# Performance work log

Measured on AMD Instinct MI355X. Metric: run time of the kernel, lower is better.

The kernel has to match this reference:

```python
import jax, jax.numpy as jnp
import numpy as np

B, S, D, H = 1, 2048, 1024, 16
DH = D // H  # 64
HID = 4 * D
EPS = 1e-5
NEG = -1.0e9


def setup_inputs() -> dict:
    key = jax.random.key(0)
    ks = jax.random.split(key, 12)
    s = 0.02
    return {
        "y": jax.random.normal(ks[0], (B, S, D), jnp.float32),
        "encoder_output": jax.random.normal(ks[1], (B, S, D), jnp.float32),
        # per-head shared projection (query_fc used for q,k,v — faithful to source bug)
        "Wq_self": jax.random.normal(ks[2], (H, D, DH), jnp.float32) * s,
        "bq_self": jax.random.normal(ks[3], (H, DH), jnp.float32) * s,
        "Wq_cross": jax.random.normal(ks[4], (H, D, DH), jnp.float32) * s,
        "bq_cross": jax.random.normal(ks[5], (H, DH), jnp.float32) * s,
        "g1": jnp.ones((D,), jnp.float32), "beta1": jnp.zeros((D,), jnp.float32),
        "g2": jnp.ones((D,), jnp.float32), "beta2": jnp.zeros((D,), jnp.float32),
        "g3": jnp.ones((D,), jnp.float32), "beta3": jnp.zeros((D,), jnp.float32),
        "w1": jax.random.normal(ks[6], (D, HID), jnp.float32) * s,
        "b1": jax.random.normal(ks[7], (HID,), jnp.float32) * s,
        "w2": jax.random.normal(ks[8], (HID, D), jnp.float32) * s,
        "b2": jax.random.normal(ks[9], (D,), jnp.float32) * s,
    }


def _layernorm(x, g, b):
    mu = jnp.mean(x, axis=-1, keepdims=True)
    var = jnp.mean((x - mu) ** 2, axis=-1, keepdims=True)
    return (x - mu) * jax.lax.rsqrt(var + EPS) * g + b


def _mha(x_q, x_kv, W, bias, causal):
    # source bug: q, k, v all use query_fc projection
    q = jnp.einsum('bsd,hde->bhse', x_q, W) + bias[None, :, None, :]
    k = jnp.einsum('bsd,hde->bhse', x_kv, W) + bias[None, :, None, :]
    v = jnp.einsum('bsd,hde->bhse', x_kv, W) + bias[None, :, None, :]
    scores = jnp.einsum('bhse,bhte->bhst', q, k) / jnp.sqrt(jnp.float32(DH))
    if causal:
        sq, sk = scores.shape[-2], scores.shape[-1]
        mask = jnp.triu(jnp.ones((sq, sk), bool), k=1)
        scores = jnp.where(mask, NEG, scores)
    p = jax.nn.softmax(scores, axis=-1)
    out = jnp.einsum('bhst,bhte->bhse', p, v)  # [B,H,S,DH]
    b, h, s, e = out.shape
    return out.transpose(0, 2, 1, 3).reshape(b, s, h * e)


def reference(y, encoder_output, Wq_self, bq_self, Wq_cross, bq_cross,
              g1, beta1, g2, beta2, g3, beta3, w1, b1, w2, b2):
    sa = _mha(y, y, Wq_self, bq_self, causal=True)
    y1 = _layernorm(y + sa, g1, beta1)
    ca = _mha(y1, encoder_output, Wq_cross, bq_cross, causal=False)
    y2 = _layernorm(y1 + ca, g2, beta2)
    ff = jnp.maximum(y2 @ w1 + b1, 0.0) @ w2 + b2
    return _layernorm(y2 + ff, g3, beta3)
```

## Files before the change

kernel.cpp:

```cpp
#include <hip/hip_runtime.h>
#include <hip/hip_bf16.h>


#define S_LEN 2048
#define DMODEL 1024
#define NHEAD 16
#define DHEAD 64
#define HIDDEN 4096

using bf16 = __hip_bfloat16;
typedef __attribute__((ext_vector_type(8))) short bf16x8;
typedef __attribute__((ext_vector_type(4))) float floatx4;

__device__ __forceinline__ void async_ld16(const void* g, void* l) {
  __builtin_amdgcn_global_load_lds(
      (const __attribute__((address_space(1))) unsigned int*)g,
      (__attribute__((address_space(3))) unsigned int*)l, 16, 0, 0);
}

__device__ __forceinline__ unsigned short f2bf_bits(float f) {
  __hip_bfloat16 b = __float2bfloat16(f);
  return *(unsigned short*)&b;
}

template <bool HEADB>
__global__ __launch_bounds__(256) void transp_bf16_kernel(
    const float* __restrict__ src0, bf16* __restrict__ dst0,
    const float* __restrict__ src1, bf16* __restrict__ dst1, int K, int N) {
  const float* src = blockIdx.z ? src1 : src0;
  bf16* dst = blockIdx.z ? dst1 : dst0;
  __shared__ float tile[32][33];
  const int tx = threadIdx.x & 31, ty = threadIdx.x >> 5;
  const int k0 = blockIdx.y * 32, n0 = blockIdx.x * 32;
#pragma unroll
  for (int i = 0; i < 4; ++i) {
    const int k = k0 + ty + i * 8;
    const int n = n0 + tx;
    size_t idx;
    if (HEADB)
      idx = (size_t)(n >> 6) * ((size_t)K * 64) + (size_t)k * 64 + (n & 63);
    else
      idx = (size_t)k * N + n;
    tile[ty + i * 8][tx] = src[idx];
  }
  __syncthreads();
#pragma unroll
  for (int i = 0; i < 4; ++i) {
    const int n = n0 + ty + i * 8;
    const int k = k0 + tx;
    dst[(size_t)n * K + k] = __float2bfloat16(tile[tx][ty + i * 8]);
  }
}

__global__ __launch_bounds__(256) void conv_bf16_kernel(
    const float* __restrict__ src0, bf16* __restrict__ dst0,
    const float* __restrict__ src1, bf16* __restrict__ dst1, int n4) {
  const float* src = blockIdx.z ? src1 : src0;
  bf16* dst = blockIdx.z ? dst1 : dst0;
  const int i = blockIdx.x * 256 + threadIdx.x;
  if (i >= n4) return;
  float4 v = ((const float4*)src)[i];
  unsigned short r[4] = {f2bf_bits(v.x), f2bf_bits(v.y), f2bf_bits(v.z), f2bf_bits(v.w)};
  ((ushort2*)dst)[i * 2] = make_ushort2(r[0], r[1]);
  ((ushort2*)dst)[i * 2 + 1] = make_ushort2(r[2], r[3]);
}

template <int BM, int BN, bool RELU, bool DUALT, typename CT>
__global__ __launch_bounds__(256) void mfma_gemm_kernel(
    const bf16* __restrict__ A0, const bf16* __restrict__ Bt0,
    const float* __restrict__ bias0, CT* __restrict__ C0,
    bf16* __restrict__ Ct0,
    const bf16* __restrict__ A1, const bf16* __restrict__ Bt1,
    const float* __restrict__ bias1, CT* __restrict__ C1,
    bf16* __restrict__ Ct1,
    int M, int N, int Kstride, int Klen) {
  const bf16* A = blockIdx.z ? A1 : A0;
  const bf16* Bt = blockIdx.z ? Bt1 : Bt0;
  const float* bias = blockIdx.z ? bias1 : bias0;
  CT* C = blockIdx.z ? C1 : C0;
  bf16* Ct = blockIdx.z ? Ct1 : Ct0;

  constexpr int MF = (BM + 31) / 32;
  constexpr int NF = BN / 32;
  __shared__ __align__(16) bf16 As[2][BM * 64];
  __shared__ __align__(16) bf16 Bs[2][BN * 64];

  const int tid = threadIdx.x;
  const int wave = tid >> 6;
  const int lane = tid & 63;
  const int m0 = blockIdx.y * BM;
  const int n0 = blockIdx.x * BN;
  const int wr = wave >> 1, wc = wave & 1;

  const int srow = tid >> 3;
  const int schunk = (tid & 7) ^ (srow & 7);
  const bf16* agp = A + (size_t)(m0 + srow) * Kstride + schunk * 8;
  const bf16* bgp = Bt + (size_t)(n0 + srow) * Kstride + schunk * 8;

  floatx4 acc[MF][NF];
#pragma unroll
  for (int i = 0; i < MF; ++i)
#pragma unroll
    for (int j = 0; j < NF; ++j) acc[i][j] = floatx4{0.f, 0.f, 0.f, 0.f};

  const int mrow = lane & 15;
  const int p0 = (((lane >> 4) ^ (mrow & 7)) << 4);
  const int p1 = p0 ^ 64;

  auto stage = [&](int buf, int kt) {
    char* al = (char*)As + buf * (BM * 128) + wave * 1024;
    char* bl = (char*)Bs + buf * (BN * 128) + wave * 1024;
#pragma unroll
    for (int i = 0; i < BM / 32; ++i)
      async_ld16(agp + (size_t)(32 * i) * Kstride + kt, al + i * 4096);
#pragma unroll
    for (int i = 0; i < BN / 32; ++i)
      async_ld16(bgp + (size_t)(32 * i) * Kstride + kt, bl + i * 4096);
  };

  stage(0, 0);
  __syncthreads();

  int cur = 0;
  for (int kt = 0; kt < Klen; kt += 64) {
    const char* abase = (const char*)As + cur * (BM * 128);
    const char* bbase = (const char*)Bs + cur * (BN * 128);
    bf16x8 af0[MF], af1[MF], bf0[NF], bf1[NF];
#pragma unroll
    for (int fi = 0; fi < MF; ++fi) {
      const char* ar = abase + (wr * (BM / 2) + fi * 16 + mrow) * 128;
      af0[fi] = *(const bf16x8*)(ar + p0);
      af1[fi] = *(const bf16x8*)(ar + p1);
    }
#pragma unroll
    for (int fj = 0; fj < NF; ++fj) {
      const char* br = bbase + (wc * (BN / 2) + fj * 16 + mrow) * 128;
      bf0[fj] = *(const bf16x8*)(br + p0);
      bf1[fj] = *(const bf16x8*)(br + p1);
    }

    if (kt + 64 < Klen) stage(cur ^ 1, kt + 64);

#pragma unroll
    for (int fi = 0; fi < MF; ++fi)
#pragma unroll
      for (int fj = 0; fj < NF; ++fj) {
        acc[fi][fj] = __builtin_amdgcn_mfma_f32_16x16x32_bf16(
            af0[fi], bf0[fj], acc[fi][fj], 0, 0, 0);
        acc[fi][fj] = __builtin_amdgcn_mfma_f32_16x16x32_bf16(
            af1[fi], bf1[fj], acc[fi][fj], 0, 0, 0);
      }

    __syncthreads();
    cur ^= 1;
  }

  const int erow = (lane >> 4) * 4;
  const int ecol = lane & 15;
#pragma unroll
  for (int fi = 0; fi < MF; ++fi) {
#pragma unroll
    for (int fj = 0; fj < NF; ++fj) {
      const int nn = n0 + wc * (BN / 2) + fj * 16 + ecol;
      const float bv = bias ? bias[nn] : 0.0f;
      const int mmb = m0 + wr * (BM / 2) + fi * 16 + erow;
      float v[4];
#pragma unroll
      for (int r = 0; r < 4; ++r) {
        v[r] = acc[fi][fj][r] + bv;
        if (RELU) v[r] = fmaxf(v[r], 0.0f);
        if constexpr (sizeof(CT) == 2)
          C[(size_t)(mmb + r) * N + nn] = (CT)__float2bfloat16(v[r]);
        else
          C[(size_t)(mmb + r) * N + nn] = (CT)v[r];
      }
      if (DUALT) {
        ushort4 pk;
        pk.x = f2bf_bits(v[0]);
        pk.y = f2bf_bits(v[1]);
        pk.z = f2bf_bits(v[2]);
        pk.w = f2bf_bits(v[3]);
        *(ushort4*)&Ct[(size_t)nn * M + mmb] = pk;
      }
    }
  }
}

__global__ __launch_bounds__(256) void mfma_attn_kernel(
    const bf16* __restrict__ Q, const bf16* __restrict__ K,
    const bf16* __restrict__ Vt,
    float* __restrict__ OA, float* __restrict__ OB,
    float* __restrict__ LA, float* __restrict__ LB, int causal) {
  __shared__ __align__(16) unsigned short Kt[2][32 * 64];
  __shared__ __align__(16) unsigned short Vs[2][64 * 32];
  __shared__ __align__(16) unsigned short Ps[4][512];

  const int tid = threadIdx.x;
  const int w = tid >> 6, lane = tid & 63;
  const int g = lane >> 4, c = lane & 15;
  const int h = blockIdx.y;
  const int qb = causal ? ((int)gridDim.x - 1 - (int)blockIdx.x)
                        : (int)blockIdx.x;
  const int q0 = qb * 64;
  const int z = blockIdx.z;
  const int qw = q0 + w * 16;
  float* Oz = z ? OB : OA;
  float* Lz = z ? LB : LA;

  const bf16* qrow = Q + (size_t)(qw + c) * DMODEL + h * DHEAD + g * 8;
  const bf16x8 qfa = *(const bf16x8*)qrow;
  const bf16x8 qfb = *(const bf16x8*)(qrow + 32);

  const int srk = tid >> 3;
  const int sck = (tid & 7) ^ (srk & 7);
  const bf16* kgp = K + (size_t)srk * DMODEL + h * DHEAD + sck * 8;
  const int srv = tid >> 2;
  const int scv = (tid & 3) ^ ((srv >> 1) & 3);
  const bf16* vgp = Vt + (size_t)(h * DHEAD + srv) * S_LEN + scv * 8;

  const int kpos0 = ((g ^ (c & 7)) << 4);
  const int kpos1 = kpos0 ^ 64;
  const int vpos = ((g ^ ((c >> 1) & 3)) << 4);
  char* pswave = (char*)Ps + w * 1024;

  floatx4 of[4];
#pragma unroll
  for (int md = 0; md < 4; ++md) of[md] = floatx4{0.f, 0.f, 0.f, 0.f};
  float lpart = 0.f;

  const int nkt = causal ? (q0 / 32 + 2) : (S_LEN / 32);

  auto stage = [&](int buf, int kt) {
    const int t0 = kt * 32;
    async_ld16(kgp + (size_t)t0 * DMODEL, (char*)Kt + buf * 4096 + w * 1024);
    async_ld16(vgp + t0, (char*)Vs + buf * 4096 + w * 1024);
  };

  stage(0, z);
  __syncthreads();

  int cur = 0;
  for (int kt = z; kt < nkt; kt += 2) {
    const int t0 = kt * 32;
    const bool act = !(causal && t0 >= qw + 16);

    bf16x8 kf00, kf01, kf10, kf11, vf0, vf1, vf2, vf3;
    if (act) {
      const char* kbase = (const char*)Kt + cur * 4096;
      const char* vbase = (const char*)Vs + cur * 4096;
      const char* kr0 = kbase + c * 128;
      const char* kr1 = kbase + (16 + c) * 128;
      kf00 = *(const bf16x8*)(kr0 + kpos0);
      kf01 = *(const bf16x8*)(kr0 + kpos1);
      kf10 = *(const bf16x8*)(kr1 + kpos0);
      kf11 = *(const bf16x8*)(kr1 + kpos1);
      vf0 = *(const bf16x8*)(vbase + (c)*64 + vpos);
      vf1 = *(const bf16x8*)(vbase + (16 + c) * 64 + vpos);
      vf2 = *(const bf16x8*)(vbase + (32 + c) * 64 + vpos);
      vf3 = *(const bf16x8*)(vbase + (48 + c) * 64 + vpos);
    }

    if (kt + 2 < nkt) stage(cur ^ 1, kt + 2);

    if (act) {
      const bool diag = causal && (t0 + 32 > qw);
#pragma unroll
      for (int jt = 0; jt < 2; ++jt) {
        floatx4 s = floatx4{0.f, 0.f, 0.f, 0.f};
        __builtin_amdgcn_s_setprio(1);
        s = __builtin_amdgcn_mfma_f32_16x16x32_bf16(jt ? kf10 : kf00, qfa, s, 0, 0, 0);
        s = __builtin_amdgcn_mfma_f32_16x16x32_bf16(jt ? kf11 : kf01, qfb, s, 0, 0, 0);
        __builtin_amdgcn_s_setprio(0);

        ushort4 pk;
        unsigned short* pp = (unsigned short*)&pk;
#pragma unroll
        for (int r = 0; r < 4; ++r) {
          float p = __expf(0.125f * s[r]);
          if (diag && (t0 + 16 * jt + 4 * g + r > qw + c)) p = 0.0f;
          lpart += p;
          pp[r] = f2bf_bits(p);
        }
        const int pb =
            c * 64 + ((((2 * jt + (g >> 1)) ^ ((c >> 1) & 3)) << 4) |
                      ((g & 1) << 3));
        *(ushort4*)(pswave + pb) = pk;
      }

      const bf16x8 pf = *(const bf16x8*)(pswave + c * 64 + vpos);
      __builtin_amdgcn_s_setprio(1);
      of[0] = __builtin_amdgcn_mfma_f32_16x16x32_bf16(vf0, pf, of[0], 0, 0, 0);
      of[1] = __builtin_amdgcn_mfma_f32_16x16x32_bf16(vf1, pf, of[1], 0, 0, 0);
      of[2] = __builtin_amdgcn_mfma_f32_16x16x32_bf16(vf2, pf, of[2], 0, 0, 0);
      of[3] = __builtin_amdgcn_mfma_f32_16x16x32_bf16(vf3, pf, of[3], 0, 0, 0);
      __builtin_amdgcn_s_setprio(0);
    }

    __syncthreads();
    cur ^= 1;
  }

  lpart += __shfl_xor(lpart, 16, 64);
  lpart += __shfl_xor(lpart, 32, 64);
  if (g == 0) Lz[(size_t)h * S_LEN + qw + c] = lpart;
  float* orow = Oz + (size_t)(qw + c) * DMODEL + h * DHEAD;
#pragma unroll
  for (int md = 0; md < 4; ++md) {
    float4 v;
    v.x = of[md][0];
    v.y = of[md][1];
    v.z = of[md][2];
    v.w = of[md][3];
    *(float4*)(orow + md * 16 + 4 * g) = v;
  }
}

template <bool DUAL, bool MERGE, bool SUM2>
__global__ __launch_bounds__(256) void add_ln_kernel(
    const float* __restrict__ X, const float* __restrict__ R,
    const float* __restrict__ R2, const float* __restrict__ bvec,
    const float* __restrict__ La, const float* __restrict__ Lb,
    const float* __restrict__ g, const float* __restrict__ beta,
    float* __restrict__ out, bf16* __restrict__ out2) {
  const int row = blockIdx.x;
  const int tid = threadIdx.x;

  float v[4];
  float s1 = 0.0f, s2 = 0.0f;
#pragma unroll
  for (int i = 0; i < 4; ++i) {
    const int c = tid + i * 256;
    float x = X[(size_t)row * DMODEL + c];
    if (MERGE) {
      const int h = c >> 6;
      const float rl =
          1.0f / (La[(size_t)h * S_LEN + row] + Lb[(size_t)h * S_LEN + row]);
      x += (R[(size_t)row * DMODEL + c] + R2[(size_t)row * DMODEL + c]) * rl;
    } else if (SUM2) {
      x += R[(size_t)row * DMODEL + c] + R2[(size_t)row * DMODEL + c] + bvec[c];
    } else {
      x += R[(size_t)row * DMODEL + c];
    }
    v[i] = x;
    s1 += x;
    s2 += x * x;
  }
#pragma unroll
  for (int off = 32; off; off >>= 1) {
    s1 += __shfl_xor(s1, off, 64);
    s2 += __shfl_xor(s2, off, 64);
  }
  __shared__ float w1s[4], w2s[4];
  const int wid = tid >> 6, lane = tid & 63;
  if (lane == 0) { w1s[wid] = s1; w2s[wid] = s2; }
  __syncthreads();
  s1 = w1s[0] + w1s[1] + w1s[2] + w1s[3];
  s2 = w2s[0] + w2s[1] + w2s[2] + w2s[3];

  const float mu = s1 * (1.0f / DMODEL);
  const float var = s2 * (1.0f / DMODEL) - mu * mu;
  const float rstd = rsqrtf(var + 1e-5f);

#pragma unroll
  for (int i = 0; i < 4; ++i) {
    const int c = tid + i * 256;
    const float r = (v[i] - mu) * rstd * g[c] + beta[c];
    out[(size_t)row * DMODEL + c] = r;
    if (DUAL) out2[(size_t)row * DMODEL + c] = __float2bfloat16(r);
  }
}

extern "C" void kernel_launch(void* const* d_in, const int* in_sizes, int n_in,
                              void* d_out, int out_size, void* d_ws, size_t ws_size,
                              hipStream_t stream) {
  const float* y      = (const float*)d_in[0];
  const float* enc    = (const float*)d_in[1];
  const float* Wself  = (const float*)d_in[2];
  const float* bself  = (const float*)d_in[3];
  const float* Wcross = (const float*)d_in[4];
  const float* bcross = (const float*)d_in[5];
  const float* g1     = (const float*)d_in[6];
  const float* be1    = (const float*)d_in[7];
  const float* g2     = (const float*)d_in[8];
  const float* be2    = (const float*)d_in[9];
  const float* g3     = (const float*)d_in[10];
  const float* be3    = (const float*)d_in[11];
  const float* w1     = (const float*)d_in[12];
  const float* b1     = (const float*)d_in[13];
  const float* w2     = (const float*)d_in[14];
  const float* b2     = (const float*)d_in[15];
  float* out = (float*)d_out;

  char* ws = (char*)d_ws;
  const size_t MB = 1024 * 1024;
  bf16*  ybf   = (bf16*)(ws + 0 * MB);
  bf16*  encbf = (bf16*)(ws + 4 * MB);
  float* PA    = (float*)(ws + 0 * MB);
  float* PB    = (float*)(ws + 8 * MB);
  float* Y1    = (float*)(ws + 16 * MB);
  float* Y2    = (float*)(ws + 24 * MB);
  bf16*  Q12b  = (bf16*)(ws + 32 * MB);
  bf16*  Q1t   = (bf16*)(ws + 36 * MB);
  bf16*  K2b   = (bf16*)(ws + 40 * MB);
  bf16*  K2t   = (bf16*)(ws + 44 * MB);
  bf16*  w1t   = (bf16*)(ws + 48 * MB);
  bf16*  w2t   = (bf16*)(ws + 56 * MB);
  bf16*  Wst   = (bf16*)(ws + 64 * MB);
  bf16*  Wct   = (bf16*)(ws + 66 * MB);
  bf16*  Y1bf  = (bf16*)(ws + 68 * MB);
  bf16*  Y2bf  = (bf16*)(ws + 72 * MB);
  float* La    = (float*)(ws + 76 * MB);
  float* Lb    = (float*)(ws + 76 * MB + 512 * 1024);
  bf16*  FFH   = (bf16*)(ws + 0 * MB);
  float* FFa   = (float*)(ws + 32 * MB);
  float* FFb   = (float*)(ws + 40 * MB);

  const dim3 blk(256);
  const dim3 gT_w(DMODEL / 32, DMODEL / 32, 2);
  const dim3 gT_w1(HIDDEN / 32, DMODEL / 32);
  const dim3 gT_w2(DMODEL / 32, HIDDEN / 32);
  const dim3 gConv(S_LEN * DMODEL / 4 / 256, 1, 2);
  const dim3 gProj2(DMODEL / 64, S_LEN / 128, 2);
  const dim3 gProj(DMODEL / 64, S_LEN / 64);
  const dim3 gFf1(HIDDEN / 128, S_LEN / 128);
  const dim3 gFf2(DMODEL / 64, S_LEN / 128, 2);
  const dim3 gAttn(S_LEN / 64, NHEAD, 2);
  const dim3 gLn(S_LEN);

  transp_bf16_kernel<true><<<gT_w, blk, 0, stream>>>(
      Wself, Wst, Wcross, Wct, DMODEL, DMODEL);
  transp_bf16_kernel<false><<<gT_w1, blk, 0, stream>>>(
      w1, w1t, nullptr, nullptr, DMODEL, HIDDEN);
  transp_bf16_kernel<false><<<gT_w2, blk, 0, stream>>>(
      w2, w2t, nullptr, nullptr, HIDDEN, DMODEL);
  conv_bf16_kernel<<<gConv, blk, 0, stream>>>(
      y, ybf, enc, encbf, S_LEN * DMODEL / 4);

  mfma_gemm_kernel<128, 64, false, true, bf16><<<gProj2, blk, 0, stream>>>(
      ybf, Wst, bself, Q12b, Q1t,
      encbf, Wct, bcross, K2b, K2t, S_LEN, DMODEL, DMODEL, DMODEL);
  mfma_attn_kernel<<<gAttn, blk, 0, stream>>>(
      Q12b, Q12b, Q1t, PA, PB, La, Lb, 1);
  add_ln_kernel<true, true, false><<<gLn, blk, 0, stream>>>(
      y, PA, PB, nullptr, La, Lb, g1, be1, Y1, Y1bf);
  mfma_gemm_kernel<64, 64, false, false, bf16><<<gProj, blk, 0, stream>>>(
      Y1bf, Wct, bcross, Q12b, nullptr,
      nullptr, nullptr, nullptr, nullptr, nullptr, S_LEN, DMODEL, DMODEL, DMODEL);
  mfma_attn_kernel<<<gAttn, blk, 0, stream>>>(
      Q12b, K2b, K2t, PA, PB, La, Lb, 0);
  add_ln_kernel<true, true, false><<<gLn, blk, 0, stream>>>(
      Y1, PA, PB, nullptr, La, Lb, g2, be2, Y2, Y2bf);
  mfma_gemm_kernel<128, 128, true, false, bf16><<<gFf1, blk, 0, stream>>>(
      Y2bf, w1t, b1, FFH, nullptr,
      nullptr, nullptr, nullptr, nullptr, nullptr, S_LEN, HIDDEN, DMODEL, DMODEL);
  mfma_gemm_kernel<128, 64, false, false, float><<<gFf2, blk, 0, stream>>>(
      FFH, w2t, nullptr, FFa, nullptr,
      FFH + HIDDEN / 2, w2t + HIDDEN / 2, nullptr, FFb, nullptr,
      S_LEN, DMODEL, HIDDEN, HIDDEN / 2);
  add_ln_kernel<false, false, true><<<gLn, blk, 0, stream>>>(
      Y2, FFa, FFb, b2, nullptr, nullptr, g3, be3, out, nullptr);
}
```

Before: 308.5 us.

## Unroll attention double-buffer loop with precomputed LDS offsets; vectorize add+LayerNorm

The attention loop is manually unrolled into two phases with constant buffer bases, so the ping-pong index goes away and the LDS offsets are hoisted out of the loop. Softmax probabilities are packed with the hardware v_cvt_pk_bf16_f32 instruction and accumulated into split partial sums. The add+LayerNorm kernel now has each thread handle four contiguous floats with float4 loads and stores instead of strided scalar accesses. Together these aim to cut address arithmetic, conversion overhead and memory transaction count, at the cost of inline asm and some code growth.

```diff
diff --git a/kernel.cpp b/kernel.cpp
--- a/kernel.cpp
+++ b/kernel.cpp
@@ -223,10 +223,19 @@
   const int vpos = ((g ^ ((c >> 1) & 3)) << 4);
   char* pswave = (char*)Ps + w * 1024;
 
-  floatx4 of[4];
-#pragma unroll
-  for (int md = 0; md < 4; ++md) of[md] = floatx4{0.f, 0.f, 0.f, 0.f};
-  float lpart = 0.f;
+  const int ko00 = c * 128 + kpos0, ko01 = c * 128 + kpos1;
+  const int ko10 = (16 + c) * 128 + kpos0, ko11 = (16 + c) * 128 + kpos1;
+  const int vo0 = c * 64 + vpos, vo1 = (16 + c) * 64 + vpos;
+  const int vo2 = (32 + c) * 64 + vpos, vo3 = (48 + c) * 64 + vpos;
+  char* const pw0 = pswave + c * 64 +
+      ((((g >> 1) ^ ((c >> 1) & 3)) << 4) | ((g & 1) << 3));
+  char* const pw1 = pswave + c * 64 +
+      ((((2 + (g >> 1)) ^ ((c >> 1) & 3)) << 4) | ((g & 1) << 3));
+  const char* const pr = pswave + vo0;
+
+  floatx4 of0{0.f, 0.f, 0.f, 0.f}, of1{0.f, 0.f, 0.f, 0.f};
+  floatx4 of2{0.f, 0.f, 0.f, 0.f}, of3{0.f, 0.f, 0.f, 0.f};
+  float lp0 = 0.f, lp1 = 0.f;
 
   const int nkt = causal ? (q0 / 32 + 2) : (S_LEN / 32);
 
@@ -236,34 +245,24 @@
     async_ld16(vgp + t0, (char*)Vs + buf * 4096 + w * 1024);
   };
 
-  stage(0, z);
-  __syncthreads();
-
-  int cur = 0;
-  for (int kt = z; kt < nkt; kt += 2) {
+  auto phase = [&](const char* kb, const char* vb, int sbuf, int kt) {
     const int t0 = kt * 32;
     const bool act = !(causal && t0 >= qw + 16);
-
     bf16x8 kf00, kf01, kf10, kf11, vf0, vf1, vf2, vf3;
     if (act) {
-      const char* kbase = (const char*)Kt + cur * 4096;
-      const char* vbase = (const char*)Vs + cur * 4096;
-      const char* kr0 = kbase + c * 128;
-      const char* kr1 = kbase + (16 + c) * 128;
-      kf00 = *(const bf16x8*)(kr0 + kpos0);
-      kf01 = *(const bf16x8*)(kr0 + kpos1);
-      kf10 = *(const bf16x8*)(kr1 + kpos0);
-      kf11 = *(const bf16x8*)(kr1 + kpos1);
-      vf0 = *(const bf16x8*)(vbase + (c)*64 + vpos);
-      vf1 = *(const bf16x8*)(vbase + (16 + c) * 64 + vpos);
-      vf2 = *(const bf16x8*)(vbase + (32 + c) * 64 + vpos);
-      vf3 = *(const bf16x8*)(vbase + (48 + c) * 64 + vpos);
+      kf00 = *(const bf16x8*)(kb + ko00);
+      kf01 = *(const bf16x8*)(kb + ko01);
+      kf10 = *(const bf16x8*)(kb + ko10);
+      kf11 = *(const bf16x8*)(kb + ko11);
+      vf0 = *(const bf16x8*)(vb + vo0);
+      vf1 = *(const bf16x8*)(vb + vo1);
+      vf2 = *(const bf16x8*)(vb + vo2);
+      vf3 = *(const bf16x8*)(vb + vo3);
     }
-
-    if (kt + 2 < nkt) stage(cur ^ 1, kt + 2);
-
+    if (kt + 2 < nkt) stage(sbuf, kt + 2);
     if (act) {
       const bool diag = causal && (t0 + 32 > qw);
+      const int qq = qw + c;
 #pragma unroll
       for (int jt = 0; jt < 2; ++jt) {
         floatx4 s = floatx4{0.f, 0.f, 0.f, 0.f};
@@ -272,46 +271,64 @@
         s = __builtin_amdgcn_mfma_f32_16x16x32_bf16(jt ? kf11 : kf01, qfb, s, 0, 0, 0);
         __builtin_amdgcn_s_setprio(0);
 
-        ushort4 pk;
-        unsigned short* pp = (unsigned short*)&pk;
-#pragma unroll
-        for (int r = 0; r < 4; ++r) {
-          float p = __expf(0.125f * s[r]);
-          if (diag && (t0 + 16 * jt + 4 * g + r > qw + c)) p = 0.0f;
-          lpart += p;
-          pp[r] = f2bf_bits(p);
+        float e0 = __expf(0.125f * s[0]);
+        float e1 = __expf(0.125f * s[1]);
+        float e2 = __expf(0.125f * s[2]);
+        float e3 = __expf(0.125f * s[3]);
+        if (diag) {
+          const int tb = t0 + 16 * jt + 4 * g;
+          if (tb + 0 > qq) e0 = 0.f;
+          if (tb + 1 > qq) e1 = 0.f;
+          if (tb + 2 > qq) e2 = 0.f;
+          if (tb + 3 > qq) e3 = 0.f;
         }
-        const int pb =
-            c * 64 + ((((2 * jt + (g >> 1)) ^ ((c >> 1) & 3)) << 4) |
-                      ((g & 1) << 3));
-        *(ushort4*)(pswave + pb) = pk;
+        lp0 += e0 + e1;
+        lp1 += e2 + e3;
+        unsigned int r01, r23;
+        asm("v_cvt_pk_bf16_f32 %0, %1, %2" : "=v"(r01) : "v"(e0), "v"(e1));
+        asm("v_cvt_pk_bf16_f32 %0, %1, %2" : "=v"(r23) : "v"(e2), "v"(e3));
+        *(uint2*)(jt ? pw1 : pw0) = make_uint2(r01, r23);
       }
 
-      const bf16x8 pf = *(const bf16x8*)(pswave + c * 64 + vpos);
+      const bf16x8 pf = *(const bf16x8*)pr;
       __builtin_amdgcn_s_setprio(1);
-      of[0] = __builtin_amdgcn_mfma_f32_16x16x32_bf16(vf0, pf, of[0], 0, 0, 0);
-      of[1] = __builtin_amdgcn_mfma_f32_16x16x32_bf16(vf1, pf, of[1], 0, 0, 0);
-      of[2] = __builtin_amdgcn_mfma_f32_16x16x32_bf16(vf2, pf, of[2], 0, 0, 0);
-      of[3] = __builtin_amdgcn_mfma_f32_16x16x32_bf16(vf3, pf, of[3], 0, 0, 0);
+      of0 = __builtin_amdgcn_mfma_f32_16x16x32_bf16(vf0, pf, of0, 0, 0, 0);
+      of1 = __builtin_amdgcn_mfma_f32_16x16x32_bf16(vf1, pf, of1, 0, 0, 0);
+      of2 = __builtin_amdgcn_mfma_f32_16x16x32_bf16(vf2, pf, of2, 0, 0, 0);
+      of3 = __builtin_amdgcn_mfma_f32_16x16x32_bf16(vf3, pf, of3, 0, 0, 0);
       __builtin_amdgcn_s_setprio(0);
     }
-
     __syncthreads();
-    cur ^= 1;
-  }
-
+  };
+
+  stage(0, z);
+  __syncthreads();
+
+  int kt = z;
+  while (true) {
+    phase((const char*)Kt, (const char*)Vs, 1, kt);
+    kt += 2;
+    if (kt >= nkt) break;
+    phase((const char*)Kt + 4096, (const char*)Vs + 4096, 0, kt);
+    kt += 2;
+    if (kt >= nkt) break;
+  }
+
+  float lpart = lp0 + lp1;
   lpart += __shfl_xor(lpart, 16, 64);
   lpart += __shfl_xor(lpart, 32, 64);
   if (g == 0) Lz[(size_t)h * S_LEN + qw + c] = lpart;
   float* orow = Oz + (size_t)(qw + c) * DMODEL + h * DHEAD;
-#pragma unroll
-  for (int md = 0; md < 4; ++md) {
+  {
     float4 v;
-    v.x = of[md][0];
-    v.y = of[md][1];
-    v.z = of[md][2];
-    v.w = of[md][3];
-    *(float4*)(orow + md * 16 + 4 * g) = v;
+    v.x = of0[0]; v.y = of0[1]; v.z = of0[2]; v.w = of0[3];
+    *(float4*)(orow + 0 * 16 + 4 * g) = v;
+    v.x = of1[0]; v.y = of1[1]; v.z = of1[2]; v.w = of1[3];
+    *(float4*)(orow + 1 * 16 + 4 * g) = v;
+    v.x = of2[0]; v.y = of2[1]; v.z = of2[2]; v.w = of2[3];
+    *(float4*)(orow + 2 * 16 + 4 * g) = v;
+    v.x = of3[0]; v.y = of3[1]; v.z = of3[2]; v.w = of3[3];
+    *(float4*)(orow + 3 * 16 + 4 * g) = v;
   }
 }
 
@@ -324,27 +341,35 @@
     float* __restrict__ out, bf16* __restrict__ out2) {
   const int row = blockIdx.x;
   const int tid = threadIdx.x;
-
-  float v[4];
-  float s1 = 0.0f, s2 = 0.0f;
-#pragma unroll
-  for (int i = 0; i < 4; ++i) {
-    const int c = tid + i * 256;
-    float x = X[(size_t)row * DMODEL + c];
-    if (MERGE) {
-      const int h = c >> 6;
-      const float rl =
-          1.0f / (La[(size_t)h * S_LEN + row] + Lb[(size_t)h * S_LEN + row]);
-      x += (R[(size_t)row * DMODEL + c] + R2[(size_t)row * DMODEL + c]) * rl;
-    } else if (SUM2) {
-      x += R[(size_t)row * DMODEL + c] + R2[(size_t)row * DMODEL + c] + bvec[c];
-    } else {
-      x += R[(size_t)row * DMODEL + c];
-    }
-    v[i] = x;
-    s1 += x;
-    s2 += x * x;
-  }
+  const int c = tid * 4;
+  const size_t base = (size_t)row * DMODEL + c;
+
+  float4 x = *(const float4*)&X[base];
+  if (MERGE) {
+    const int h = c >> 6;
+    const float rl =
+        1.0f / (La[(size_t)h * S_LEN + row] + Lb[(size_t)h * S_LEN + row]);
+    const float4 r = *(const float4*)&R[base];
+    const float4 r2 = *(const float4*)&R2[base];
+    x.x += (r.x + r2.x) * rl;
+    x.y += (r.y + r2.y) * rl;
+    x.z += (r.z + r2.z) * rl;
+    x.w += (r.w + r2.w) * rl;
+  } else if (SUM2) {
+    const float4 r = *(const float4*)&R[base];
+    const float4 r2 = *(const float4*)&R2[base];
+    const float4 bv = *(const float4*)&bvec[c];
+    x.x += r.x + r2.x + bv.x;
+    x.y += r.y + r2.y + bv.y;
+    x.z += r.z + r2.z + bv.z;
+    x.w += r.w + r2.w + bv.w;
+  } else {
+    const float4 r = *(const float4*)&R[base];
+    x.x += r.x; x.y += r.y; x.z += r.z; x.w += r.w;
+  }
+  float s1 = x.x + x.y + x.z + x.w;
+  float s2 = x.x * x.x + x.y * x.y + x.z * x.z + x.w * x.w;
+
 #pragma unroll
   for (int off = 32; off; off >>= 1) {
     s1 += __shfl_xor(s1, off, 64);
@@ -361,12 +386,21 @@
   const float var = s2 * (1.0f / DMODEL) - mu * mu;
   const float rstd = rsqrtf(var + 1e-5f);
 
-#pragma unroll
-  for (int i = 0; i < 4; ++i) {
-    const int c = tid + i * 256;
-    const float r = (v[i] - mu) * rstd * g[c] + beta[c];
-    out[(size_t)row * DMODEL + c] = r;
-    if (DUAL) out2[(size_t)row * DMODEL + c] = __float2bfloat16(r);
+  const float4 gg = *(const float4*)&g[c];
+  const float4 bb = *(const float4*)&beta[c];
+  float4 r;
+  r.x = (x.x - mu) * rstd * gg.x + bb.x;
+  r.y = (x.y - mu) * rstd * gg.y + bb.y;
+  r.z = (x.z - mu) * rstd * gg.z + bb.z;
+  r.w = (x.w - mu) * rstd * gg.w + bb.w;
+  *(float4*)&out[base] = r;
+  if (DUAL) {
+    ushort4 pk;
+    pk.x = f2bf_bits(r.x);
+    pk.y = f2bf_bits(r.y);
+    pk.z = f2bf_bits(r.z);
+    pk.w = f2bf_bits(r.w);
+    *(ushort4*)&out2[base] = pk;
   }
 }
 
```

After: 292.9 us. 5.0% less time.
